# Kernel tuning notes

Hardware: AMD Instinct MI355X
Metric: run time of the kernel (lower is better)

## Reference

```python
import jax, jax.numpy as jnp
import numpy as np

B, H, W, NUM_CLASSES = 128, 224, 224, 1000
EPS = 1e-6


def setup_inputs() -> dict:
    key = jax.random.key(0)
    k1, k2, k3, k4, k5, k6 = jax.random.split(key, 6)
    # objects are probabilities fed straight to BCE -> keep strictly in (0,1)
    objects = jnp.clip(jax.random.uniform(k1, (B, H, W)), EPS, 1.0 - EPS)
    scores = jax.random.normal(k2, (B, NUM_CLASSES), dtype=jnp.float32)
    locs = jax.random.normal(k3, (B, 4, H, W), dtype=jnp.float32)
    label = jax.random.randint(k4, (B,), 0, NUM_CLASSES)
    obj_mask = (jax.random.uniform(k5, (B, H, W)) < 0.05).astype(jnp.float32)
    coords = jax.random.uniform(k6, (B, 4, H, W), dtype=jnp.float32)
    gt = jnp.concatenate([obj_mask[:, None], coords], axis=1)  # [B,5,H,W]
    return {
        "objects": objects,
        "scores": scores,
        "locs": locs,
        "label": label,
        "gt": gt,
        "obj_coor": jnp.float32(5.0),
        "no_obj_confi": jnp.float32(0.5),
        "img_class_weight": jnp.float32(1.0),
    }


def reference(objects, scores, locs, label, gt, obj_coor, no_obj_confi, img_class_weight):
    gt0 = gt[:, 0]                      # [B,H,W] objectness target in {0,1}
    obj_m = gt0 == 1.0
    noobj_m = gt0 == 0.0
    # BCE terms; clamp logs at -100 like torch's binary_cross_entropy
    log_p = jnp.maximum(jnp.log(objects), -100.0)
    log_1mp = jnp.maximum(jnp.log1p(-objects), -100.0)
    no_obj_confi_loss = jnp.sum(jnp.where(noobj_m, -log_1mp, 0.0))
    obj_confi_loss = jnp.sum(jnp.where(obj_m, -log_p, 0.0))
    # masked coordinate L2: sum over 4 coord channels at object cells
    sq = jnp.sum((locs - gt[:, 1:5]) ** 2, axis=1)  # [B,H,W]
    obj_coor_loss = jnp.sum(jnp.where(obj_m, sq, 0.0))
    # image-level classification: mean cross entropy
    logz = jax.nn.log_softmax(scores, axis=-1)
    img_class_loss = -jnp.mean(jnp.take_along_axis(logz, label[:, None], axis=1))
    batch_size = objects.shape[0]
    return img_class_weight * img_class_loss + (
        no_obj_confi * no_obj_confi_loss + obj_confi_loss + obj_coor * obj_coor_loss
    ) / batch_size
```

## Files before the change

kernel.cpp:

```cpp
#include <hip/hip_runtime.h>
#include <math.h>

#define HW4  12544
#define BATCH 128
#define NUM_CLASSES 1000
#define N4   (BATCH * HW4)
#define G    2
#define TPB  256
#define NTHREADS (N4 / G)
#define NBLOCKS  (NTHREADS / TPB)

typedef float v4f __attribute__((ext_vector_type(4)));


__launch_bounds__(TPB, 4)
__global__ void pixel_loss_kernel(const v4f* __restrict__ objects,
                                  const v4f* __restrict__ locs,
                                  const v4f* __restrict__ gt,
                                  const float* __restrict__ obj_coor_p,
                                  const float* __restrict__ no_obj_confi_p,
                                  float* __restrict__ ws) {
    const float coorW = *obj_coor_p;
    const float noW   = *no_obj_confi_p;

    const unsigned tid = blockIdx.x * TPB + threadIdx.x;

    v4f o[G], m4[G], gc[G][4], lc[G][4];
#pragma unroll
    for (int k = 0; k < G; ++k) {
        const unsigned g   = tid + (unsigned)(k * NTHREADS);
        const unsigned b   = g / HW4;
        const unsigned hw4 = g - b * HW4;
        const unsigned gtb = b * (5 * HW4) + hw4;
        const unsigned lcb = b * (4 * HW4) + hw4;

        o[k]  = objects[g];
        m4[k] = gt[gtb];
#pragma unroll
        for (int c = 0; c < 4; ++c) {
            gc[k][c] = gt[gtb + (unsigned)((1 + c) * HW4)];
            lc[k][c] = locs[lcb + (unsigned)(c * HW4)];
        }
    }

    asm volatile(""
        : "+v"(o[0]),     "+v"(o[1]),
          "+v"(m4[0]),    "+v"(m4[1]),
          "+v"(gc[0][0]), "+v"(gc[0][1]), "+v"(gc[0][2]), "+v"(gc[0][3]),
          "+v"(gc[1][0]), "+v"(gc[1][1]), "+v"(gc[1][2]), "+v"(gc[1][3]),
          "+v"(lc[0][0]), "+v"(lc[0][1]), "+v"(lc[0][2]), "+v"(lc[0][3]),
          "+v"(lc[1][0]), "+v"(lc[1][1]), "+v"(lc[1][2]), "+v"(lc[1][3]));

    float acc = 0.0f;
#pragma unroll
    for (int k = 0; k < G; ++k) {
        v4f sq = {0.f, 0.f, 0.f, 0.f};
#pragma unroll
        for (int c = 0; c < 4; ++c) {
            v4f d = lc[k][c] - gc[k][c];
            sq += d * d;
        }
#pragma unroll
        for (int j = 0; j < 4; ++j) {
            const float p = o[k][j];
            const float m = m4[k][j];
            const float lognop = fmaxf(__logf(1.0f - p), -100.0f);
            const float logp   = fmaxf(__logf(p), -100.0f);
            const float a = -noW * lognop;
            const float b = fmaf(coorW, sq[j], -logp);
            acc += fmaf(m, b - a, a);
        }
    }

#pragma unroll
    for (int off = 32; off > 0; off >>= 1)
        acc += __shfl_down(acc, off, 64);

    __shared__ float smem[4];
    const int lane = threadIdx.x & 63;
    const int wave = threadIdx.x >> 6;
    if (lane == 0) smem[wave] = acc;
    __syncthreads();
    if (threadIdx.x == 0) {
        atomicAdd(&ws[0], smem[0] + smem[1] + smem[2] + smem[3]);
    }
}

__global__ void class_loss_kernel(const float* __restrict__ scores,
                                  const int* __restrict__ label,
                                  float* __restrict__ ws) {
    const int b = blockIdx.x;
    const float* row = scores + b * NUM_CLASSES;

    __shared__ float red[4];
    __shared__ float s_bcast;
    const int lane = threadIdx.x & 63;
    const int wave = threadIdx.x >> 6;

    float mx = -INFINITY;
    for (int i = threadIdx.x; i < NUM_CLASSES; i += blockDim.x)
        mx = fmaxf(mx, row[i]);
#pragma unroll
    for (int off = 32; off > 0; off >>= 1)
        mx = fmaxf(mx, __shfl_down(mx, off, 64));
    if (lane == 0) red[wave] = mx;
    __syncthreads();
    if (threadIdx.x == 0)
        s_bcast = fmaxf(fmaxf(red[0], red[1]), fmaxf(red[2], red[3]));
    __syncthreads();
    mx = s_bcast;

    float se = 0.0f;
    for (int i = threadIdx.x; i < NUM_CLASSES; i += blockDim.x)
        se += __expf(row[i] - mx);
#pragma unroll
    for (int off = 32; off > 0; off >>= 1)
        se += __shfl_down(se, off, 64);
    __syncthreads();
    if (lane == 0) red[wave] = se;
    __syncthreads();
    if (threadIdx.x == 0) {
        float lse = mx + logf(red[0] + red[1] + red[2] + red[3]);
        atomicAdd(&ws[1], -(row[label[b]] - lse));
    }
}

__global__ void finalize_kernel(const float* __restrict__ ws,
                                const float* __restrict__ img_class_weight_p,
                                float* __restrict__ out) {
    if (threadIdx.x == 0 && blockIdx.x == 0) {
        float img_class_loss = ws[1] / (float)BATCH;
        out[0] = img_class_weight_p[0] * img_class_loss + ws[0] / (float)BATCH;
    }
}

extern "C" void kernel_launch(void* const* d_in, const int* in_sizes, int n_in,
                              void* d_out, int out_size, void* d_ws, size_t ws_size,
                              hipStream_t stream) {
    const float* objects = (const float*)d_in[0];
    const float* scores  = (const float*)d_in[1];
    const float* locs    = (const float*)d_in[2];
    const int*   label   = (const int*)d_in[3];
    const float* gt      = (const float*)d_in[4];
    const float* obj_coor         = (const float*)d_in[5];
    const float* no_obj_confi     = (const float*)d_in[6];
    const float* img_class_weight = (const float*)d_in[7];

    float* ws  = (float*)d_ws;
    float* out = (float*)d_out;

    hipMemsetAsync(ws, 0, 2 * sizeof(float), stream);

    pixel_loss_kernel<<<NBLOCKS, TPB, 0, stream>>>(
        (const v4f*)objects, (const v4f*)locs, (const v4f*)gt,
        obj_coor, no_obj_confi, ws);

    class_loss_kernel<<<BATCH, 256, 0, stream>>>(scores, label, ws);

    finalize_kernel<<<1, 64, 0, stream>>>(ws, img_class_weight, out);
}
```

Measured before the change: 283.7 us.

## Fuse pixel, class, and finalize kernels; stream coords via global_load_lds double buffering

Merges the three kernels into one launch. The first 128 blocks compute the per-row log-softmax cross entropy, and the remaining blocks handle pixels. The last block to finish, found through an atomic counter, writes the final output. The pixel path now loops over 4 chunks per block and double-buffers the 8 coordinate streams into LDS with direct global-to-LDS loads and manual vmcnt waits. This removes two launch gaps and aims to overlap memory latency. The cost is hand-tuned waitcnt values that must match the load count, plus larger LDS use (64KB per block), which limits occupancy.

Result: slower. 362.5 us (+27.8%).

```diff
diff --git a/kernel.cpp b/kernel.cpp
--- a/kernel.cpp
+++ b/kernel.cpp
@@ -1,136 +1,154 @@
 #include <hip/hip_runtime.h>
 #include <math.h>
 
-#define HW4  12544
+#define HW4   12544
 #define BATCH 128
 #define NUM_CLASSES 1000
-#define N4   (BATCH * HW4)
-#define G    2
-#define TPB  256
-#define NTHREADS (N4 / G)
-#define NBLOCKS  (NTHREADS / TPB)
+#define N4    (BATCH * HW4)
+#define TPB   256
+#define S     4
+#define PIXBLOCKS (N4 / (TPB * S))
+#define CPB   (HW4 / TPB)
+#define GRID  (PIXBLOCKS + BATCH)
 
 typedef float v4f __attribute__((ext_vector_type(4)));
 
+__device__ __forceinline__ void gl_lds16(const v4f* g, v4f* l) {
+    __builtin_amdgcn_global_load_lds(
+        (const __attribute__((address_space(1))) void*)g,
+        (__attribute__((address_space(3))) void*)l,
+        16, 0, 0);
+}
 
-__launch_bounds__(TPB, 4)
-__global__ void pixel_loss_kernel(const v4f* __restrict__ objects,
+__launch_bounds__(TPB, 2)
+__global__ void fused_loss_kernel(const v4f* __restrict__ objects,
                                   const v4f* __restrict__ locs,
                                   const v4f* __restrict__ gt,
+                                  const float* __restrict__ scores,
+                                  const int*   __restrict__ label,
                                   const float* __restrict__ obj_coor_p,
                                   const float* __restrict__ no_obj_confi_p,
-                                  float* __restrict__ ws) {
-    const float coorW = *obj_coor_p;
-    const float noW   = *no_obj_confi_p;
+                                  const float* __restrict__ img_class_weight_p,
+                                  float* __restrict__ ws,
+                                  float* __restrict__ out) {
+    __shared__ v4f lds[2][8][TPB];
+    const int tid  = threadIdx.x;
+    const int lane = tid & 63;
+    const int wave = tid >> 6;
 
-    const unsigned tid = blockIdx.x * TPB + threadIdx.x;
+    if (blockIdx.x < BATCH) {
+        const int b = blockIdx.x;
+        const float* row = scores + b * NUM_CLASSES;
+        float* red = (float*)lds;
 
-    v4f o[G], m4[G], gc[G][4], lc[G][4];
+        float mx = -INFINITY;
+        for (int i = tid; i < NUM_CLASSES; i += TPB)
+            mx = fmaxf(mx, row[i]);
 #pragma unroll
-    for (int k = 0; k < G; ++k) {
-        const unsigned g   = tid + (unsigned)(k * NTHREADS);
-        const unsigned b   = g / HW4;
-        const unsigned hw4 = g - b * HW4;
-        const unsigned gtb = b * (5 * HW4) + hw4;
-        const unsigned lcb = b * (4 * HW4) + hw4;
+        for (int off = 32; off > 0; off >>= 1)
+            mx = fmaxf(mx, __shfl_down(mx, off, 64));
+        if (lane == 0) red[wave] = mx;
+        __syncthreads();
+        if (tid == 0)
+            red[4] = fmaxf(fmaxf(red[0], red[1]), fmaxf(red[2], red[3]));
+        __syncthreads();
+        mx = red[4];
 
-        o[k]  = objects[g];
-        m4[k] = gt[gtb];
+        float se = 0.0f;
+        for (int i = tid; i < NUM_CLASSES; i += TPB)
+            se += __expf(row[i] - mx);
 #pragma unroll
-        for (int c = 0; c < 4; ++c) {
-            gc[k][c] = gt[gtb + (unsigned)((1 + c) * HW4)];
-            lc[k][c] = locs[lcb + (unsigned)(c * HW4)];
+        for (int off = 32; off > 0; off >>= 1)
+            se += __shfl_down(se, off, 64);
+        __syncthreads();
+        if (lane == 0) red[wave] = se;
+        __syncthreads();
+        if (tid == 0) {
+            float lse = mx + logf(red[0] + red[1] + red[2] + red[3]);
+            atomicAdd(&ws[1], -(row[label[b]] - lse));
         }
+    } else {
+        float coorW = *obj_coor_p;
+        float noW   = *no_obj_confi_p;
+        asm volatile("" : "+v"(coorW), "+v"(noW));
+        asm volatile("s_waitcnt vmcnt(0)" ::: "memory");
+
+        const unsigned c0 = (blockIdx.x - BATCH) * S;
+        v4f o_r[2], m_r[2];
+
+        auto issue = [&](int s, int buf) {
+            const unsigned c  = c0 + (unsigned)s;
+            const unsigned b  = c / CPB;
+            const unsigned hw = (c - b * CPB) * TPB + tid;
+            const v4f* gtp = gt   + (size_t)b * (5 * HW4) + hw;
+            const v4f* lcp = locs + (size_t)b * (4 * HW4) + hw;
+            o_r[buf] = objects[(size_t)b * HW4 + hw];
+            m_r[buf] = gtp[0];
+            v4f* dst0 = &lds[buf][0][wave << 6];
+            gl_lds16(gtp + 1 * HW4, &lds[buf][0][wave << 6]);
+            gl_lds16(gtp + 2 * HW4, &lds[buf][1][wave << 6]);
+            gl_lds16(gtp + 3 * HW4, &lds[buf][2][wave << 6]);
+            gl_lds16(gtp + 4 * HW4, &lds[buf][3][wave << 6]);
+            gl_lds16(lcp + 0 * HW4, &lds[buf][4][wave << 6]);
+            gl_lds16(lcp + 1 * HW4, &lds[buf][5][wave << 6]);
+            gl_lds16(lcp + 2 * HW4, &lds[buf][6][wave << 6]);
+            gl_lds16(lcp + 3 * HW4, &lds[buf][7][wave << 6]);
+            (void)dst0;
+        };
+
+        issue(0, 0);
+        float acc = 0.0f;
+#pragma unroll
+        for (int s = 0; s < S; ++s) {
+            const int buf = s & 1;
+            if (s + 1 < S) {
+                issue(s + 1, buf ^ 1);
+                asm volatile("s_waitcnt vmcnt(10)" ::: "memory");
+            } else {
+                asm volatile("s_waitcnt vmcnt(0)" ::: "memory");
+            }
+            v4f sq = {0.f, 0.f, 0.f, 0.f};
+#pragma unroll
+            for (int j = 0; j < 4; ++j) {
+                v4f g = lds[buf][j][tid];
+                v4f l = lds[buf][4 + j][tid];
+                v4f d = l - g;
+                sq += d * d;
+            }
+            const v4f o = o_r[buf], m = m_r[buf];
+#pragma unroll
+            for (int j = 0; j < 4; ++j) {
+                const float p  = o[j];
+                const float mm = m[j];
+                const float lognop = fmaxf(__logf(1.0f - p), -100.0f);
+                const float logp   = fmaxf(__logf(p),        -100.0f);
+                const float a  = -noW * lognop;
+                const float bb = fmaf(coorW, sq[j], -logp);
+                acc += fmaf(mm, bb - a, a);
+            }
+        }
+
+#pragma unroll
+        for (int off = 32; off > 0; off >>= 1)
+            acc += __shfl_down(acc, off, 64);
+        __syncthreads();
+        float* red = (float*)lds;
+        if (lane == 0) red[wave] = acc;
+        __syncthreads();
+        if (tid == 0)
+            atomicAdd(&ws[0], red[0] + red[1] + red[2] + red[3]);
     }
 
-    asm volatile(""
-        : "+v"(o[0]),     "+v"(o[1]),
-          "+v"(m4[0]),    "+v"(m4[1]),
-          "+v"(gc[0][0]), "+v"(gc[0][1]), "+v"(gc[0][2]), "+v"(gc[0][3]),
-          "+v"(gc[1][0]), "+v"(gc[1][1]), "+v"(gc[1][2]), "+v"(gc[1][3]),
-          "+v"(lc[0][0]), "+v"(lc[0][1]), "+v"(lc[0][2]), "+v"(lc[0][3]),
-          "+v"(lc[1][0]), "+v"(lc[1][1]), "+v"(lc[1][2]), "+v"(lc[1][3]));
-
-    float acc = 0.0f;
-#pragma unroll
-    for (int k = 0; k < G; ++k) {
-        v4f sq = {0.f, 0.f, 0.f, 0.f};
-#pragma unroll
-        for (int c = 0; c < 4; ++c) {
-            v4f d = lc[k][c] - gc[k][c];
-            sq += d * d;
+    if (tid == 0) {
+        __threadfence();
+        unsigned done = atomicAdd((unsigned int*)&ws[2], 1u);
+        if (done == (unsigned)(GRID - 1)) {
+            __threadfence();
+            const float pix = atomicAdd(&ws[0], 0.0f);
+            const float cls = atomicAdd(&ws[1], 0.0f);
+            out[0] = img_class_weight_p[0] * (cls / (float)BATCH)
+                   + pix / (float)BATCH;
         }
-#pragma unroll
-        for (int j = 0; j < 4; ++j) {
-            const float p = o[k][j];
-            const float m = m4[k][j];
-            const float lognop = fmaxf(__logf(1.0f - p), -100.0f);
-            const float logp   = fmaxf(__logf(p), -100.0f);
-            const float a = -noW * lognop;
-            const float b = fmaf(coorW, sq[j], -logp);
-            acc += fmaf(m, b - a, a);
-        }
-    }
-
-#pragma unroll
-    for (int off = 32; off > 0; off >>= 1)
-        acc += __shfl_down(acc, off, 64);
-
-    __shared__ float smem[4];
-    const int lane = threadIdx.x & 63;
-    const int wave = threadIdx.x >> 6;
-    if (lane == 0) smem[wave] = acc;
-    __syncthreads();
-    if (threadIdx.x == 0) {
-        atomicAdd(&ws[0], smem[0] + smem[1] + smem[2] + smem[3]);
-    }
-}
-
-__global__ void class_loss_kernel(const float* __restrict__ scores,
-                                  const int* __restrict__ label,
-                                  float* __restrict__ ws) {
-    const int b = blockIdx.x;
-    const float* row = scores + b * NUM_CLASSES;
-
-    __shared__ float red[4];
-    __shared__ float s_bcast;
-    const int lane = threadIdx.x & 63;
-    const int wave = threadIdx.x >> 6;
-
-    float mx = -INFINITY;
-    for (int i = threadIdx.x; i < NUM_CLASSES; i += blockDim.x)
-        mx = fmaxf(mx, row[i]);
-#pragma unroll
-    for (int off = 32; off > 0; off >>= 1)
-        mx = fmaxf(mx, __shfl_down(mx, off, 64));
-    if (lane == 0) red[wave] = mx;
-    __syncthreads();
-    if (threadIdx.x == 0)
-        s_bcast = fmaxf(fmaxf(red[0], red[1]), fmaxf(red[2], red[3]));
-    __syncthreads();
-    mx = s_bcast;
-
-    float se = 0.0f;
-    for (int i = threadIdx.x; i < NUM_CLASSES; i += blockDim.x)
-        se += __expf(row[i] - mx);
-#pragma unroll
-    for (int off = 32; off > 0; off >>= 1)
-        se += __shfl_down(se, off, 64);
-    __syncthreads();
-    if (lane == 0) red[wave] = se;
-    __syncthreads();
-    if (threadIdx.x == 0) {
-        float lse = mx + logf(red[0] + red[1] + red[2] + red[3]);
-        atomicAdd(&ws[1], -(row[label[b]] - lse));
-    }
-}
-
-__global__ void finalize_kernel(const float* __restrict__ ws,
-                                const float* __restrict__ img_class_weight_p,
-                                float* __restrict__ out) {
-    if (threadIdx.x == 0 && blockIdx.x == 0) {
-        float img_class_loss = ws[1] / (float)BATCH;
-        out[0] = img_class_weight_p[0] * img_class_loss + ws[0] / (float)BATCH;
     }
 }
 
@@ -149,13 +167,9 @@
     float* ws  = (float*)d_ws;
     float* out = (float*)d_out;
 
-    hipMemsetAsync(ws, 0, 2 * sizeof(float), stream);
+    hipMemsetAsync(ws, 0, 3 * sizeof(float), stream);
 
-    pixel_loss_kernel<<<NBLOCKS, TPB, 0, stream>>>(
+    fused_loss_kernel<<<GRID, TPB, 0, stream>>>(
         (const v4f*)objects, (const v4f*)locs, (const v4f*)gt,
-        obj_coor, no_obj_confi, ws);
-
-    class_loss_kernel<<<BATCH, 256, 0, stream>>>(scores, label, ws);
-
-    finalize_kernel<<<1, 64, 0, stream>>>(ws, img_class_weight, out);
+        scores, label, obj_coor, no_obj_confi, img_class_weight, ws, out);
 }
```
